# Kernel optimization log

Hardware: AMD Instinct MI355X
Metric: run time of the kernel (lower is better)

Reference implementation:

```python
import jax, jax.numpy as jnp
import numpy as np

EPS = 1e-6
N_NODES = 50000
N_EDGES = 800000
IN_DIM = 128
OUT_DIM = 128
HEADS = 4
D_K = OUT_DIM // HEADS
ATT_DIM = 2 * D_K + 1  # use_edge_feat=True


def setup_inputs() -> dict:
    key = jax.random.key(0)
    ks = jax.random.split(key, 8)
    h = jax.random.normal(ks[0], (N_NODES, IN_DIM), dtype=jnp.float32)
    edge_index = jax.random.randint(ks[1], (2, N_EDGES), 0, N_NODES, dtype=jnp.int64)
    edge_feat = jax.random.normal(ks[2], (N_EDGES, 1), dtype=jnp.float32)
    # parameters
    W_w = jax.random.normal(ks[3], (OUT_DIM, IN_DIM), dtype=jnp.float32) / np.sqrt(IN_DIM)
    W_b = jnp.zeros((OUT_DIM,), dtype=jnp.float32)
    att = jax.random.normal(ks[4], (HEADS, ATT_DIM), dtype=jnp.float32)
    ln_g = jnp.ones((OUT_DIM,), dtype=jnp.float32)
    ln_b = jnp.zeros((OUT_DIM,), dtype=jnp.float32)
    return {"h": h, "edge_index": edge_index, "edge_feat": edge_feat,
            "W_w": W_w, "W_b": W_b, "att": att, "ln_g": ln_g, "ln_b": ln_b}


def _layer_norm(x, g, b):
    mu = jnp.mean(x, axis=-1, keepdims=True)
    var = jnp.mean(jnp.square(x - mu), axis=-1, keepdims=True)
    return (x - mu) * jax.lax.rsqrt(var + 1e-5) * g + b


def reference(h, edge_index, edge_feat, W_w, W_b, att, ln_g, ln_b):
    num_nodes = h.shape[0]
    z = h @ W_w.T + W_b                      # [N, out_dim]
    zr = z.reshape(num_nodes, HEADS, D_K)    # [N, H, d_k]
    src, dst = edge_index[0], edge_index[1]
    h_s = zr[src]                            # [E, H, d_k]
    h_d = zr[dst]                            # [E, H, d_k]
    f_e = jnp.broadcast_to(edge_feat[:, None, :], (edge_feat.shape[0], HEADS, 1))
    concat = jnp.concatenate([h_s, h_d, f_e], axis=-1)  # [E, H, att_dim]
    scores = jnp.sum(concat * att[None], axis=-1)        # [E, H]
    scores = jnp.where(scores >= 0, scores, 0.2 * scores)  # LeakyReLU(0.2)
    scores = jnp.clip(scores, -20.0, 20.0)
    alpha = jnp.exp(scores)                               # [E, H]
    denom = jax.ops.segment_sum(alpha, dst, num_segments=num_nodes)  # [N, H]
    norm_alpha = alpha / (denom[dst] + EPS)               # [E, H]
    weighted = h_s * norm_alpha[..., None]                # [E, H, d_k]
    out = jax.ops.segment_sum(weighted, dst, num_segments=num_nodes)  # [N, H, d_k]
    out = out.reshape(num_nodes, OUT_DIM) + z
    out = _layer_norm(out, ln_g, ln_b)
    return jax.nn.elu(out)
```

## Files before the change

### kernel.cpp

```cpp
#include <hip/hip_runtime.h>
#include <hip/hip_bf16.h>
#include <math.h>

typedef __attribute__((ext_vector_type(8))) short bf16x8;
typedef __attribute__((ext_vector_type(4))) float f32x4;

__device__ __forceinline__ unsigned short f2bf(float f) {
    unsigned u = __float_as_uint(f);
    unsigned r = ((u >> 16) & 1u) + 0x7fffu;
    return (unsigned short)((u + r) >> 16);
}
__device__ __forceinline__ float bf2f(unsigned short s) {
    return __uint_as_float((unsigned)s << 16);
}
__device__ __forceinline__ float bfL(unsigned u) { return __uint_as_float(u << 16); }
__device__ __forceinline__ float bfH(unsigned u) { return __uint_as_float(u & 0xffff0000u); }

__global__ __launch_bounds__(256) void k_prep(const float* __restrict__ W,
                                              const float* __restrict__ bias,
                                              const float* __restrict__ att,
                                              unsigned short* __restrict__ Wb16,
                                              unsigned short* __restrict__ wsdB,
                                              float* __restrict__ consts,
                                              int* __restrict__ head4, int N) {
    const int t = threadIdx.x;
    const int bid = blockIdx.x;
    if (bid == 0) {
#pragma unroll
        for (int q = 0; q < 8; ++q) {
            int gi = q * 256 + t;
            int kg = gi >> 7, row = gi & 127;
            int kbase = (kg >> 2) * 32 + (kg & 3) * 4;
            unsigned pk[4];
#pragma unroll
            for (int p = 0; p < 4; ++p) {
                int e0 = 2 * p, e1 = 2 * p + 1;
                float v0 = W[(size_t)row * 128 + kbase + (e0 >> 2) * 16 + (e0 & 3)];
                float v1 = W[(size_t)row * 128 + kbase + (e1 >> 2) * 16 + (e1 & 3)];
                pk[p] = ((unsigned)f2bf(v1) << 16) | f2bf(v0);
            }
            *reinterpret_cast<uint4*>(&Wb16[(size_t)gi * 8]) =
                make_uint4(pk[0], pk[1], pk[2], pk[3]);
        }
    } else if (bid == 1) {
        int kg = t >> 4, la = t & 15;
        int hd = la & 3;
        int isDst = (la >> 2) & 1;
        int isLo = la >> 3;
        unsigned short vals[8];
#pragma unroll
        for (int e = 0; e < 8; ++e) {
            int k = (kg >> 2) * 32 + (e >> 2) * 16 + (kg & 3) * 4 + (e & 3);
            float w = 0.f;
            for (int j = 0; j < 32; ++j)
                w += W[(size_t)(hd * 32 + j) * 128 + k] * att[hd * 65 + isDst * 32 + j];
            unsigned short hi = f2bf(w);
            vals[e] = isLo ? f2bf(w - bf2f(hi)) : hi;
        }
        int gi = kg * 16 + la;
        unsigned pk[4];
#pragma unroll
        for (int p = 0; p < 4; ++p)
            pk[p] = ((unsigned)vals[2 * p + 1] << 16) | vals[2 * p];
        *reinterpret_cast<uint4*>(&wsdB[(size_t)gi * 8]) =
            make_uint4(pk[0], pk[1], pk[2], pk[3]);
        if (t < 8) {
            int chd = t & 3, cIsD = t >> 2;
            float c = 0.f;
            for (int j = 0; j < 32; ++j)
                c += bias[chd * 32 + j] * att[chd * 65 + cIsD * 32 + j];
            consts[t] = c;
        }
    } else {
        int i = ((bid - 2) * 256 + t) * 4;
        if (i < N * 4)
            *reinterpret_cast<int4*>(&head4[i]) = make_int4(-1, -1, -1, -1);
    }
}

__global__ __launch_bounds__(256) void k_mega(
        const float* __restrict__ h, const unsigned short* __restrict__ Wb16,
        const unsigned short* __restrict__ wsdB, const float* __restrict__ consts,
        const float* __restrict__ bias,
        unsigned short* __restrict__ zb16,
        float* __restrict__ s_src, float* __restrict__ s_dst, int N) {
    __shared__ short hS[16 * 64 * 8];
    const int t = threadIdx.x;
    const int by = blockIdx.x & 1;
    const int n0 = (blockIdx.x >> 1) * 64;
    const int obase = by * 64;

#pragma unroll
    for (int q = 0; q < 8; ++q) {
        int f = q * 256 + t;
        int nd = f >> 5;
        int k4 = (f & 31) * 4;
        int ks = k4 >> 5, rr = k4 & 31;
        int half = rr >> 4, g = (rr & 15) >> 2;
        int kg = ks * 4 + g;
        int slot = kg * 64 + (nd ^ (kg & 7));
        int hn = n0 + nd; if (hn > N - 1) hn = N - 1;
        float4 v = *reinterpret_cast<const float4*>(&h[(size_t)hn * 128 + k4]);
        uint2 pk = make_uint2(((unsigned)f2bf(v.y) << 16) | f2bf(v.x),
                              ((unsigned)f2bf(v.w) << 16) | f2bf(v.z));
        *reinterpret_cast<uint2*>(&hS[slot * 8 + half * 4]) = pk;
    }
    __syncthreads();

    const int wv = t >> 6, l = t & 63;
    const int la = l & 15, lb = l >> 4;
    const int nbase = wv * 16;
    const int node = n0 + nbase + la;

    bf16x8 hfr[4];
#pragma unroll
    for (int ks = 0; ks < 4; ++ks) {
        int kg = ks * 4 + lb;
        int slot = kg * 64 + ((nbase + la) ^ (kg & 7));
        hfr[ks] = *reinterpret_cast<const bf16x8*>(&hS[slot * 8]);
    }

    if (by == 0) {
        f32x4 accS = {0.f, 0.f, 0.f, 0.f};
#pragma unroll
        for (int ks = 0; ks < 4; ++ks) {
            int kg = ks * 4 + lb;
            bf16x8 sfr = *reinterpret_cast<const bf16x8*>(&wsdB[(size_t)(kg * 16 + la) * 8]);
            accS = __builtin_amdgcn_mfma_f32_16x16x32_bf16(sfr, hfr[ks], accS, 0, 0, 0);
        }
        float t0 = accS[0] + __shfl_xor(accS[0], 32);
        float t1 = accS[1] + __shfl_xor(accS[1], 32);
        float t2 = accS[2] + __shfl_xor(accS[2], 32);
        float t3 = accS[3] + __shfl_xor(accS[3], 32);
        if (lb < 2 && node < N) {
            float4 cv = *reinterpret_cast<const float4*>(&consts[lb * 4]);
            float4 o = make_float4(t0 + cv.x, t1 + cv.y, t2 + cv.z, t3 + cv.w);
            float* dp = (lb == 0) ? s_src : s_dst;
            *reinterpret_cast<float4*>(&dp[(size_t)node * 4]) = o;
        }
    }

#pragma unroll
    for (int ot = 0; ot < 4; ++ot) {
        f32x4 acc = {0.f, 0.f, 0.f, 0.f};
#pragma unroll
        for (int ks = 0; ks < 4; ++ks) {
            int kg = ks * 4 + lb;
            bf16x8 wfr = *reinterpret_cast<const bf16x8*>(
                &Wb16[((size_t)kg * 128 + obase + ot * 16 + la) * 8]);
            acc = __builtin_amdgcn_mfma_f32_16x16x32_bf16(wfr, hfr[ks], acc, 0, 0, 0);
        }
        int colb = obase + ot * 16 + lb * 4;
        float4 bq = *reinterpret_cast<const float4*>(&bias[colb]);
        if (node < N) {
            uint2 pk = make_uint2(
                ((unsigned)f2bf(acc[1] + bq.y) << 16) | f2bf(acc[0] + bq.x),
                ((unsigned)f2bf(acc[3] + bq.w) << 16) | f2bf(acc[2] + bq.z));
            *reinterpret_cast<uint2*>(&zb16[(size_t)node * 128 + colb]) = pk;
        }
    }
}

__global__ __launch_bounds__(256) void k_edge(const int* __restrict__ src,
                                              const int* __restrict__ dst,
                                              const float* __restrict__ ef,
                                              const float* __restrict__ att,
                                              const float* __restrict__ s_src,
                                              const float* __restrict__ s_dst,
                                              int* __restrict__ head4,
                                              int4* __restrict__ epkt, int E) {
    int e = blockIdx.x * 256 + threadIdx.x;
    if (e >= E) return;
    int s = src[e], d = dst[e];
    float fv = ef[e];
    float4 ss = *reinterpret_cast<const float4*>(&s_src[(size_t)s * 4]);
    float4 sd = *reinterpret_cast<const float4*>(&s_dst[(size_t)d * 4]);
    float aE0 = att[64], aE1 = att[129], aE2 = att[194], aE3 = att[259];
    float sc0 = ss.x + sd.x + fv * aE0;
    float sc1 = ss.y + sd.y + fv * aE1;
    float sc2 = ss.z + sd.z + fv * aE2;
    float sc3 = ss.w + sd.w + fv * aE3;
    sc0 = sc0 >= 0.f ? sc0 : 0.2f * sc0;  sc1 = sc1 >= 0.f ? sc1 : 0.2f * sc1;
    sc2 = sc2 >= 0.f ? sc2 : 0.2f * sc2;  sc3 = sc3 >= 0.f ? sc3 : 0.2f * sc3;
    float a0 = expf(fminf(fmaxf(sc0, -20.f), 20.f));
    float a1 = expf(fminf(fmaxf(sc1, -20.f), 20.f));
    float a2 = expf(fminf(fmaxf(sc2, -20.f), 20.f));
    float a3 = expf(fminf(fmaxf(sc3, -20.f), 20.f));
    int prev = atomicExch(&head4[(size_t)d * 4 + (e & 3)], e);
    epkt[e] = make_int4(s, prev,
        (int)(((unsigned)f2bf(a1) << 16) | f2bf(a0)),
        (int)(((unsigned)f2bf(a3) << 16) | f2bf(a2)));
}

__global__ __launch_bounds__(256) void k_agg_final(const int* __restrict__ head4,
                                                   const int4* __restrict__ epkt,
                                                   const uint4* __restrict__ zb4,
                                                   const float* __restrict__ g,
                                                   const float* __restrict__ bparm,
                                                   float* __restrict__ out, int N) {
    int wave = threadIdx.x >> 6, lane = threadIdx.x & 63;
    int l16 = lane & 15;
    int n = blockIdx.x * 16 + wave * 4 + (lane >> 4);
    if (n >= N) return;
    const int hd = l16 >> 2;
    int4 eh = *reinterpret_cast<const int4*>(&head4[(size_t)n * 4]);
    int e0 = eh.x, e1 = eh.y, e2 = eh.z, e3 = eh.w;
    float A0 = 0.f, A1 = 0.f, A2 = 0.f, A3 = 0.f;
    float A4 = 0.f, A5 = 0.f, A6 = 0.f, A7 = 0.f;
    float da = 0.f;
#define UNPK(P, AV) { unsigned u = (hd & 2) ? (unsigned)(P).w : (unsigned)(P).z; \
    AV = (hd & 1) ? bfH(u) : bfL(u); }
#define STEP(EV) if (EV != -1) { \
        int4 p = epkt[EV]; \
        uint4 q = zb4[(size_t)p.x * 16 + l16]; \
        float a; UNPK(p, a) \
        A0 += bfL(q.x) * a; A1 += bfH(q.x) * a; \
        A2 += bfL(q.y) * a; A3 += bfH(q.y) * a; \
        A4 += bfL(q.z) * a; A5 += bfH(q.z) * a; \
        A6 += bfL(q.w) * a; A7 += bfH(q.w) * a; \
        da += a; EV = p.y; }
    while (((e0 & e1) & (e2 & e3)) != -1) {
        STEP(e0) STEP(e1) STEP(e2) STEP(e3)
    }
#undef STEP
#undef UNPK

    float inv = 1.f / (da + 1e-6f);
    uint4 qz = zb4[(size_t)n * 16 + l16];
    float x0 = A0 * inv + bfL(qz.x);
    float x1 = A1 * inv + bfH(qz.x);
    float x2 = A2 * inv + bfL(qz.y);
    float x3 = A3 * inv + bfH(qz.y);
    float x4 = A4 * inv + bfL(qz.z);
    float x5 = A5 * inv + bfH(qz.z);
    float x6 = A6 * inv + bfL(qz.w);
    float x7 = A7 * inv + bfH(qz.w);
    float s = ((x0 + x1) + (x2 + x3)) + ((x4 + x5) + (x6 + x7));
#pragma unroll
    for (int off = 1; off < 16; off <<= 1) s += __shfl_xor(s, off);
    float mu = s * (1.f / 128.f);
    float d0 = x0 - mu, d1 = x1 - mu, d2 = x2 - mu, d3 = x3 - mu;
    float d4 = x4 - mu, d5 = x5 - mu, d6 = x6 - mu, d7 = x7 - mu;
    float q = ((d0 * d0 + d1 * d1) + (d2 * d2 + d3 * d3))
            + ((d4 * d4 + d5 * d5) + (d6 * d6 + d7 * d7));
#pragma unroll
    for (int off = 1; off < 16; off <<= 1) q += __shfl_xor(q, off);
    float rstd = rsqrtf(q * (1.f / 128.f) + 1e-5f);
    const int c = l16 * 8;
    float4 g0 = *reinterpret_cast<const float4*>(&g[c]);
    float4 g1 = *reinterpret_cast<const float4*>(&g[c + 4]);
    float4 b0 = *reinterpret_cast<const float4*>(&bparm[c]);
    float4 b1 = *reinterpret_cast<const float4*>(&bparm[c + 4]);
    float y0 = d0 * rstd * g0.x + b0.x;
    float y1 = d1 * rstd * g0.y + b0.y;
    float y2 = d2 * rstd * g0.z + b0.z;
    float y3 = d3 * rstd * g0.w + b0.w;
    float y4 = d4 * rstd * g1.x + b1.x;
    float y5 = d5 * rstd * g1.y + b1.y;
    float y6 = d6 * rstd * g1.z + b1.z;
    float y7 = d7 * rstd * g1.w + b1.w;
    y0 = y0 > 0.f ? y0 : expf(y0) - 1.f;
    y1 = y1 > 0.f ? y1 : expf(y1) - 1.f;
    y2 = y2 > 0.f ? y2 : expf(y2) - 1.f;
    y3 = y3 > 0.f ? y3 : expf(y3) - 1.f;
    y4 = y4 > 0.f ? y4 : expf(y4) - 1.f;
    y5 = y5 > 0.f ? y5 : expf(y5) - 1.f;
    y6 = y6 > 0.f ? y6 : expf(y6) - 1.f;
    y7 = y7 > 0.f ? y7 : expf(y7) - 1.f;
    *reinterpret_cast<float4*>(&out[(size_t)n * 128 + c]) = make_float4(y0, y1, y2, y3);
    *reinterpret_cast<float4*>(&out[(size_t)n * 128 + c + 4]) = make_float4(y4, y5, y6, y7);
}

extern "C" void kernel_launch(void* const* d_in, const int* in_sizes, int n_in,
                              void* d_out, int out_size, void* d_ws, size_t ws_size,
                              hipStream_t stream) {
    const float* h   = (const float*)d_in[0];
    const int*   ei  = (const int*)d_in[1];
    const float* ef  = (const float*)d_in[2];
    const float* Ww  = (const float*)d_in[3];
    const float* Wb  = (const float*)d_in[4];
    const float* att = (const float*)d_in[5];
    const float* lng = (const float*)d_in[6];
    const float* lnb = (const float*)d_in[7];
    float* out = (float*)d_out;

    const int N = in_sizes[0] / 128;
    const int E = in_sizes[1] / 2;
    const int* src = ei;
    const int* dst = ei + E;

    char* ws = (char*)d_ws;
    unsigned short* zb16   = (unsigned short*)ws; ws += (size_t)N * 128 * 2;
    unsigned short* Wb16   = (unsigned short*)ws; ws += (size_t)128 * 128 * 2;
    unsigned short* wsdB   = (unsigned short*)ws; ws += (size_t)16 * 16 * 8 * 2;
    float*          consts = (float*)ws;          ws += (size_t)8 * 4;
    float*          s_src  = (float*)ws;          ws += (size_t)N * 4 * 4;
    float*          s_dst  = (float*)ws;          ws += (size_t)N * 4 * 4;
    int*            head4  = (int*)ws;            ws += (size_t)N * 4 * 4;
    int4*           epkt   = (int4*)ws;           ws += (size_t)E * 16;

    const int zeroBlocks = (N * 4 + 1023) / 1024;
    k_prep<<<2 + zeroBlocks, 256, 0, stream>>>(Ww, Wb, att, Wb16, wsdB, consts, head4, N);

    const int gemmBlocks = ((N + 63) / 64) * 2;
    k_mega<<<gemmBlocks, 256, 0, stream>>>(
        h, Wb16, wsdB, consts, Wb, zb16, s_src, s_dst, N);
    k_edge<<<(E + 255) / 256, 256, 0, stream>>>(src, dst, ef, att, s_src, s_dst,
                                                head4, epkt, E);
    k_agg_final<<<(N + 15) / 16, 256, 0, stream>>>(head4, epkt,
                                                   (const uint4*)zb16, lng, lnb, out, N);
}
```

Measured before the change: 128.3 us.

## Move score projection into prep and co-schedule GEMM with edge pass

Per-node attention score projections (s_src/s_dst) are now computed in fp32 in the prep kernel. Each score block rebuilds the folded W·att vectors in shared memory and dots them with h. This lets the GEMM blocks and the edge-scoring/linked-list blocks run together in one launch, removing a kernel boundary and serialization. The per-destination linked lists are also split into 8 chains instead of 4, giving more independent loads per node during aggregation. The cost is that every score block recomputes the W·att fold (redundant work), plus an extra fp32 read of h.

```diff
diff --git a/kernel.cpp b/kernel.cpp
--- a/kernel.cpp
+++ b/kernel.cpp
@@ -10,19 +10,20 @@
     unsigned r = ((u >> 16) & 1u) + 0x7fffu;
     return (unsigned short)((u + r) >> 16);
 }
-__device__ __forceinline__ float bf2f(unsigned short s) {
-    return __uint_as_float((unsigned)s << 16);
-}
 __device__ __forceinline__ float bfL(unsigned u) { return __uint_as_float(u << 16); }
 __device__ __forceinline__ float bfH(unsigned u) { return __uint_as_float(u & 0xffff0000u); }
+
+#define SCORE_NPB 32
 
 __global__ __launch_bounds__(256) void k_prep(const float* __restrict__ W,
                                               const float* __restrict__ bias,
                                               const float* __restrict__ att,
+                                              const float* __restrict__ h,
                                               unsigned short* __restrict__ Wb16,
-                                              unsigned short* __restrict__ wsdB,
-                                              float* __restrict__ consts,
-                                              int* __restrict__ head4, int N) {
+                                              float* __restrict__ s_src,
+                                              float* __restrict__ s_dst,
+                                              int* __restrict__ head8,
+                                              int N, int scoreBlocks) {
     const int t = threadIdx.x;
     const int bid = blockIdx.x;
     if (bid == 0) {
@@ -42,54 +43,104 @@
             *reinterpret_cast<uint4*>(&Wb16[(size_t)gi * 8]) =
                 make_uint4(pk[0], pk[1], pk[2], pk[3]);
         }
-    } else if (bid == 1) {
-        int kg = t >> 4, la = t & 15;
-        int hd = la & 3;
-        int isDst = (la >> 2) & 1;
-        int isLo = la >> 3;
-        unsigned short vals[8];
-#pragma unroll
-        for (int e = 0; e < 8; ++e) {
-            int k = (kg >> 2) * 32 + (e >> 2) * 16 + (kg & 3) * 4 + (e & 3);
+    } else if (bid <= scoreBlocks) {
+        __shared__ float wsdL[2][4][128];
+        __shared__ float cs[8];
+#pragma unroll
+        for (int q = 0; q < 4; ++q) {
+            int idx = q * 256 + t;
+            int isD = idx >> 9, rem = idx & 511;
+            int hd = rem >> 7, k = rem & 127;
             float w = 0.f;
             for (int j = 0; j < 32; ++j)
-                w += W[(size_t)(hd * 32 + j) * 128 + k] * att[hd * 65 + isDst * 32 + j];
-            unsigned short hi = f2bf(w);
-            vals[e] = isLo ? f2bf(w - bf2f(hi)) : hi;
-        }
-        int gi = kg * 16 + la;
-        unsigned pk[4];
-#pragma unroll
-        for (int p = 0; p < 4; ++p)
-            pk[p] = ((unsigned)vals[2 * p + 1] << 16) | vals[2 * p];
-        *reinterpret_cast<uint4*>(&wsdB[(size_t)gi * 8]) =
-            make_uint4(pk[0], pk[1], pk[2], pk[3]);
+                w += W[(size_t)(hd * 32 + j) * 128 + k] * att[hd * 65 + isD * 32 + j];
+            wsdL[isD][hd][k] = w;
+        }
         if (t < 8) {
             int chd = t & 3, cIsD = t >> 2;
             float c = 0.f;
             for (int j = 0; j < 32; ++j)
                 c += bias[chd * 32 + j] * att[chd * 65 + cIsD * 32 + j];
-            consts[t] = c;
+            cs[t] = c;
+        }
+        __syncthreads();
+        int node = (bid - 1) * SCORE_NPB + (t >> 3);
+        int p = t & 7;
+        if (node < N) {
+            const float* hp = h + (size_t)node * 128 + p * 16;
+            float ss[4] = {0.f, 0.f, 0.f, 0.f}, sd[4] = {0.f, 0.f, 0.f, 0.f};
+#pragma unroll
+            for (int q = 0; q < 4; ++q) {
+                float4 hv = *reinterpret_cast<const float4*>(hp + q * 4);
+#pragma unroll
+                for (int hd = 0; hd < 4; ++hd) {
+                    const float* wa = &wsdL[0][hd][p * 16 + q * 4];
+                    const float* wb = &wsdL[1][hd][p * 16 + q * 4];
+                    ss[hd] += hv.x * wa[0] + hv.y * wa[1] + hv.z * wa[2] + hv.w * wa[3];
+                    sd[hd] += hv.x * wb[0] + hv.y * wb[1] + hv.z * wb[2] + hv.w * wb[3];
+                }
+            }
+#pragma unroll
+            for (int off = 1; off < 8; off <<= 1)
+#pragma unroll
+                for (int hd = 0; hd < 4; ++hd) {
+                    ss[hd] += __shfl_xor(ss[hd], off);
+                    sd[hd] += __shfl_xor(sd[hd], off);
+                }
+            if (p == 0) {
+                *reinterpret_cast<float4*>(&s_src[(size_t)node * 4]) =
+                    make_float4(ss[0] + cs[0], ss[1] + cs[1], ss[2] + cs[2], ss[3] + cs[3]);
+                *reinterpret_cast<float4*>(&s_dst[(size_t)node * 4]) =
+                    make_float4(sd[0] + cs[4], sd[1] + cs[5], sd[2] + cs[6], sd[3] + cs[7]);
+            }
         }
     } else {
-        int i = ((bid - 2) * 256 + t) * 4;
-        if (i < N * 4)
-            *reinterpret_cast<int4*>(&head4[i]) = make_int4(-1, -1, -1, -1);
-    }
-}
-
-__global__ __launch_bounds__(256) void k_mega(
+        int i = ((bid - 1 - scoreBlocks) * 256 + t) * 4;
+        if (i < N * 8)
+            *reinterpret_cast<int4*>(&head8[i]) = make_int4(-1, -1, -1, -1);
+    }
+}
+
+__global__ __launch_bounds__(256) void k_work(
         const float* __restrict__ h, const unsigned short* __restrict__ Wb16,
-        const unsigned short* __restrict__ wsdB, const float* __restrict__ consts,
-        const float* __restrict__ bias,
-        unsigned short* __restrict__ zb16,
-        float* __restrict__ s_src, float* __restrict__ s_dst, int N) {
+        const float* __restrict__ bias, unsigned short* __restrict__ zb16,
+        const int* __restrict__ src, const int* __restrict__ dst,
+        const float* __restrict__ ef, const float* __restrict__ att,
+        const float* __restrict__ s_src, const float* __restrict__ s_dst,
+        int* __restrict__ head8, int4* __restrict__ epkt,
+        int N, int E, int gemmBlocks) {
     __shared__ short hS[16 * 64 * 8];
     const int t = threadIdx.x;
-    const int by = blockIdx.x & 1;
-    const int n0 = (blockIdx.x >> 1) * 64;
+    const int bid = blockIdx.x;
+
+    if (bid >= gemmBlocks) {
+        int e = (bid - gemmBlocks) * 256 + t;
+        if (e >= E) return;
+        int s = src[e], d = dst[e];
+        float fv = ef[e];
+        float4 ss = *reinterpret_cast<const float4*>(&s_src[(size_t)s * 4]);
+        float4 sd = *reinterpret_cast<const float4*>(&s_dst[(size_t)d * 4]);
+        float aE0 = att[64], aE1 = att[129], aE2 = att[194], aE3 = att[259];
+        float sc0 = ss.x + sd.x + fv * aE0;
+        float sc1 = ss.y + sd.y + fv * aE1;
+        float sc2 = ss.z + sd.z + fv * aE2;
+        float sc3 = ss.w + sd.w + fv * aE3;
+        sc0 = sc0 >= 0.f ? sc0 : 0.2f * sc0;  sc1 = sc1 >= 0.f ? sc1 : 0.2f * sc1;
+        sc2 = sc2 >= 0.f ? sc2 : 0.2f * sc2;  sc3 = sc3 >= 0.f ? sc3 : 0.2f * sc3;
+        float a0 = expf(fminf(fmaxf(sc0, -20.f), 20.f));
+        float a1 = expf(fminf(fmaxf(sc1, -20.f), 20.f));
+        float a2 = expf(fminf(fmaxf(sc2, -20.f), 20.f));
+        float a3 = expf(fminf(fmaxf(sc3, -20.f), 20.f));
+        int prev = atomicExch(&head8[(size_t)d * 8 + (e & 7)], e);
+        epkt[e] = make_int4(s, prev,
+            (int)(((unsigned)f2bf(a1) << 16) | f2bf(a0)),
+            (int)(((unsigned)f2bf(a3) << 16) | f2bf(a2)));
+        return;
+    }
+
+    const int by = bid & 1;
+    const int n0 = (bid >> 1) * 64;
     const int obase = by * 64;
-
 #pragma unroll
     for (int q = 0; q < 8; ++q) {
         int f = q * 256 + t;
@@ -120,26 +171,6 @@
         hfr[ks] = *reinterpret_cast<const bf16x8*>(&hS[slot * 8]);
     }
 
-    if (by == 0) {
-        f32x4 accS = {0.f, 0.f, 0.f, 0.f};
-#pragma unroll
-        for (int ks = 0; ks < 4; ++ks) {
-            int kg = ks * 4 + lb;
-            bf16x8 sfr = *reinterpret_cast<const bf16x8*>(&wsdB[(size_t)(kg * 16 + la) * 8]);
-            accS = __builtin_amdgcn_mfma_f32_16x16x32_bf16(sfr, hfr[ks], accS, 0, 0, 0);
-        }
-        float t0 = accS[0] + __shfl_xor(accS[0], 32);
-        float t1 = accS[1] + __shfl_xor(accS[1], 32);
-        float t2 = accS[2] + __shfl_xor(accS[2], 32);
-        float t3 = accS[3] + __shfl_xor(accS[3], 32);
-        if (lb < 2 && node < N) {
-            float4 cv = *reinterpret_cast<const float4*>(&consts[lb * 4]);
-            float4 o = make_float4(t0 + cv.x, t1 + cv.y, t2 + cv.z, t3 + cv.w);
-            float* dp = (lb == 0) ? s_src : s_dst;
-            *reinterpret_cast<float4*>(&dp[(size_t)node * 4]) = o;
-        }
-    }
-
 #pragma unroll
     for (int ot = 0; ot < 4; ++ot) {
         f32x4 acc = {0.f, 0.f, 0.f, 0.f};
@@ -161,38 +192,7 @@
     }
 }
 
-__global__ __launch_bounds__(256) void k_edge(const int* __restrict__ src,
-                                              const int* __restrict__ dst,
-                                              const float* __restrict__ ef,
-                                              const float* __restrict__ att,
-                                              const float* __restrict__ s_src,
-                                              const float* __restrict__ s_dst,
-                                              int* __restrict__ head4,
-                                              int4* __restrict__ epkt, int E) {
-    int e = blockIdx.x * 256 + threadIdx.x;
-    if (e >= E) return;
-    int s = src[e], d = dst[e];
-    float fv = ef[e];
-    float4 ss = *reinterpret_cast<const float4*>(&s_src[(size_t)s * 4]);
-    float4 sd = *reinterpret_cast<const float4*>(&s_dst[(size_t)d * 4]);
-    float aE0 = att[64], aE1 = att[129], aE2 = att[194], aE3 = att[259];
-    float sc0 = ss.x + sd.x + fv * aE0;
-    float sc1 = ss.y + sd.y + fv * aE1;
-    float sc2 = ss.z + sd.z + fv * aE2;
-    float sc3 = ss.w + sd.w + fv * aE3;
-    sc0 = sc0 >= 0.f ? sc0 : 0.2f * sc0;  sc1 = sc1 >= 0.f ? sc1 : 0.2f * sc1;
-    sc2 = sc2 >= 0.f ? sc2 : 0.2f * sc2;  sc3 = sc3 >= 0.f ? sc3 : 0.2f * sc3;
-    float a0 = expf(fminf(fmaxf(sc0, -20.f), 20.f));
-    float a1 = expf(fminf(fmaxf(sc1, -20.f), 20.f));
-    float a2 = expf(fminf(fmaxf(sc2, -20.f), 20.f));
-    float a3 = expf(fminf(fmaxf(sc3, -20.f), 20.f));
-    int prev = atomicExch(&head4[(size_t)d * 4 + (e & 3)], e);
-    epkt[e] = make_int4(s, prev,
-        (int)(((unsigned)f2bf(a1) << 16) | f2bf(a0)),
-        (int)(((unsigned)f2bf(a3) << 16) | f2bf(a2)));
-}
-
-__global__ __launch_bounds__(256) void k_agg_final(const int* __restrict__ head4,
+__global__ __launch_bounds__(256) void k_agg_final(const int* __restrict__ head8,
                                                    const int4* __restrict__ epkt,
                                                    const uint4* __restrict__ zb4,
                                                    const float* __restrict__ g,
@@ -203,8 +203,10 @@
     int n = blockIdx.x * 16 + wave * 4 + (lane >> 4);
     if (n >= N) return;
     const int hd = l16 >> 2;
-    int4 eh = *reinterpret_cast<const int4*>(&head4[(size_t)n * 4]);
-    int e0 = eh.x, e1 = eh.y, e2 = eh.z, e3 = eh.w;
+    int4 eha = *reinterpret_cast<const int4*>(&head8[(size_t)n * 8]);
+    int4 ehb = *reinterpret_cast<const int4*>(&head8[(size_t)n * 8 + 4]);
+    int e0 = eha.x, e1 = eha.y, e2 = eha.z, e3 = eha.w;
+    int e4 = ehb.x, e5 = ehb.y, e6 = ehb.z, e7 = ehb.w;
     float A0 = 0.f, A1 = 0.f, A2 = 0.f, A3 = 0.f;
     float A4 = 0.f, A5 = 0.f, A6 = 0.f, A7 = 0.f;
     float da = 0.f;
@@ -219,8 +221,9 @@
         A4 += bfL(q.z) * a; A5 += bfH(q.z) * a; \
         A6 += bfL(q.w) * a; A7 += bfH(q.w) * a; \
         da += a; EV = p.y; }
-    while (((e0 & e1) & (e2 & e3)) != -1) {
+    while ((((e0 & e1) & (e2 & e3)) & ((e4 & e5) & (e6 & e7))) != -1) {
         STEP(e0) STEP(e1) STEP(e2) STEP(e3)
+        STEP(e4) STEP(e5) STEP(e6) STEP(e7)
     }
 #undef STEP
 #undef UNPK
@@ -292,21 +295,21 @@
     char* ws = (char*)d_ws;
     unsigned short* zb16   = (unsigned short*)ws; ws += (size_t)N * 128 * 2;
     unsigned short* Wb16   = (unsigned short*)ws; ws += (size_t)128 * 128 * 2;
-    unsigned short* wsdB   = (unsigned short*)ws; ws += (size_t)16 * 16 * 8 * 2;
-    float*          consts = (float*)ws;          ws += (size_t)8 * 4;
     float*          s_src  = (float*)ws;          ws += (size_t)N * 4 * 4;
     float*          s_dst  = (float*)ws;          ws += (size_t)N * 4 * 4;
-    int*            head4  = (int*)ws;            ws += (size_t)N * 4 * 4;
+    int*            head8  = (int*)ws;            ws += (size_t)N * 8 * 4;
     int4*           epkt   = (int4*)ws;           ws += (size_t)E * 16;
 
-    const int zeroBlocks = (N * 4 + 1023) / 1024;
-    k_prep<<<2 + zeroBlocks, 256, 0, stream>>>(Ww, Wb, att, Wb16, wsdB, consts, head4, N);
+    const int scoreBlocks = (N + SCORE_NPB - 1) / SCORE_NPB;
+    const int headBlocks  = (N * 8 / 4 + 255) / 256;
+    k_prep<<<1 + scoreBlocks + headBlocks, 256, 0, stream>>>(
+        Ww, Wb, att, h, Wb16, s_src, s_dst, head8, N, scoreBlocks);
 
     const int gemmBlocks = ((N + 63) / 64) * 2;
-    k_mega<<<gemmBlocks, 256, 0, stream>>>(
-        h, Wb16, wsdB, consts, Wb, zb16, s_src, s_dst, N);
-    k_edge<<<(E + 255) / 256, 256, 0, stream>>>(src, dst, ef, att, s_src, s_dst,
-                                                head4, epkt, E);
-    k_agg_final<<<(N + 15) / 16, 256, 0, stream>>>(head4, epkt,
+    const int edgeBlocks = (E + 255) / 256;
+    k_work<<<gemmBlocks + edgeBlocks, 256, 0, stream>>>(
+        h, Wb16, Wb, zb16, src, dst, ef, att, s_src, s_dst, head8, epkt,
+        N, E, gemmBlocks);
+    k_agg_final<<<(N + 15) / 16, 256, 0, stream>>>(head8, epkt,
                                                    (const uint4*)zb16, lng, lnb, out, N);
 }
```

After: 125.5 us. 1.02x faster.
